# Performance work log

Measured on AMD Instinct MI355X. Metric: run time of the kernel, lower is better.

## Reference

```python
import jax, jax.numpy as jnp
import numpy as np

N_NODES = 100000
N_EDGES = 1600000
NUM_FEATURES = 128
NUM_CLASSES = 10
NUM_GRAPHS = 64


def setup_inputs() -> dict:
    key = jax.random.key(0)
    ks = jax.random.split(key, 16)
    x = jax.random.normal(ks[0], (N_NODES, NUM_FEATURES), dtype=jnp.float32)
    edge_index = jax.random.randint(ks[1], (2, N_EDGES), 0, N_NODES, dtype=jnp.int64)
    batch = jnp.sort(jax.random.randint(ks[2], (N_NODES,), 0, NUM_GRAPHS, dtype=jnp.int64))

    def glorot(k, fan_in, fan_out):
        s = jnp.sqrt(6.0 / (fan_in + fan_out)).astype(jnp.float32)
        return jax.random.uniform(k, (fan_in, fan_out), jnp.float32, -s, s)

    dims = [(NUM_FEATURES, 128), (128, 128), (128, 128), (128, 64), (64, 32)]
    params = {}
    for i, (fi, fo) in enumerate(dims, start=1):
        params[f"W{i}"] = glorot(ks[2 + i], fi, fo)
        params[f"b{i}"] = jnp.zeros((fo,), jnp.float32)
    params["Wfc"] = glorot(ks[10], 32, NUM_CLASSES)
    params["bfc"] = jnp.zeros((NUM_CLASSES,), jnp.float32)
    return {"x": x, "edge_index": edge_index, "batch": batch, **params}


def reference(x, edge_index, batch, W1, b1, W2, b2, W3, b3, W4, b4, W5, b5, Wfc, bfc):
    N = x.shape[0]
    loops = jnp.arange(N, dtype=edge_index.dtype)
    src = jnp.concatenate([edge_index[0], loops])  # message source j
    dst = jnp.concatenate([edge_index[1], loops])  # message target i
    # GCN symmetric normalization: deg computed on targets incl. self loops
    deg = jax.ops.segment_sum(jnp.ones_like(dst, x.dtype), dst, num_segments=N)
    dinv = jnp.where(deg > 0, jax.lax.rsqrt(deg), 0.0)
    norm = (dinv[src] * dinv[dst])[:, None]  # [E+N, 1]

    def gcn_conv(h, W, b):
        h = h @ W  # transform first (smaller gather width when out < in)
        msg = h[src] * norm
        return jax.ops.segment_sum(msg, dst, num_segments=N) + b

    h = jax.nn.relu(gcn_conv(x, W1, b1))
    h = jax.nn.relu(gcn_conv(h, W2, b2))
    h = jax.nn.relu(gcn_conv(h, W3, b3))
    h = jax.nn.relu(gcn_conv(h, W4, b4))
    h = jax.nn.relu(gcn_conv(h, W5, b5))

    # global_mean_pool over graph membership
    sums = jax.ops.segment_sum(h, batch, num_segments=NUM_GRAPHS)
    cnts = jax.ops.segment_sum(jnp.ones((N,), h.dtype), batch, num_segments=NUM_GRAPHS)
    pooled = sums / jnp.maximum(cnts, 1.0)[:, None]

    # dropout is identity in eval mode
    return pooled @ Wfc + bfc
```

## Files before the change

### kernel.cpp

```cpp
#include <hip/hip_runtime.h>
#include <hip/hip_bf16.h>

#define N_NODES 100000
#define N_EDGES 1600000
#define N_GRAPHS 64
#define WNB 192
#define BCAP 64

typedef __attribute__((ext_vector_type(8))) short bf16x8;
typedef __attribute__((ext_vector_type(4))) float f32x4;

__device__ inline float bflo(unsigned u) { return __uint_as_float(u << 16); }
__device__ inline float bfhi(unsigned u) { return __uint_as_float(u & 0xffff0000u); }
__device__ inline unsigned short f2bf(float f) {
    unsigned u = __float_as_uint(f);
    return (unsigned short)((u + 0x7fff + ((u >> 16) & 1)) >> 16);
}


__global__ __launch_bounds__(256) void k_setup(int* __restrict__ cursor, int n,
                                               const float* __restrict__ W1,
                                               const float* __restrict__ W2,
                                               const float* __restrict__ W3,
                                               const float* __restrict__ W4,
                                               const float* __restrict__ W5,
                                               unsigned short* __restrict__ wt1,
                                               unsigned short* __restrict__ wt2,
                                               unsigned short* __restrict__ wt3,
                                               unsigned short* __restrict__ wt4,
                                               unsigned short* __restrict__ wt5) {
    const int nb = (N_NODES + 255) / 256;
    if ((int)blockIdx.x < nb) {
        int i = blockIdx.x * 256 + threadIdx.x;
        if (i < n) cursor[i] = i * BCAP;
        return;
    }
    int i = (blockIdx.x - nb) * 256 + threadIdx.x;
    const float* W; unsigned short* WT; int FI, FO, j;
    if (i < 16384)      { W = W1; WT = wt1; FI = 128; FO = 128; j = i; }
    else if (i < 32768) { W = W2; WT = wt2; FI = 128; FO = 128; j = i - 16384; }
    else if (i < 49152) { W = W3; WT = wt3; FI = 128; FO = 128; j = i - 32768; }
    else if (i < 57344) { W = W4; WT = wt4; FI = 128; FO = 64;  j = i - 49152; }
    else if (i < 59392) { W = W5; WT = wt5; FI = 64;  FO = 32;  j = i - 57344; }
    else return;
    int n_ = j / FI, k_ = j % FI;
    WT[j] = f2bf(W[(size_t)k_ * FO + n_]);
}


__global__ __launch_bounds__(256) void k_fillw(const int* __restrict__ ei,
                                               int* __restrict__ cursor,
                                               int* __restrict__ cols, int e) {
    const int w = blockIdx.x & 7;
    const int b = blockIdx.x >> 3;
    const int lo = w * 12500, hi = lo + 12500;
    const int4* d4 = (const int4*)(ei + e);
    const int n4 = e >> 2;
    for (int i = b * 256 + threadIdx.x; i < n4; i += WNB * 256) {
        int4 d = d4[i];
        int base = 4 * i;
        if (d.x >= lo && d.x < hi) {
            int p = atomicAdd(&cursor[d.x], 1);
            if (p < d.x * BCAP + BCAP) cols[p] = ei[base];
        }
        if (d.y >= lo && d.y < hi) {
            int p = atomicAdd(&cursor[d.y], 1);
            if (p < d.y * BCAP + BCAP) cols[p] = ei[base + 1];
        }
        if (d.z >= lo && d.z < hi) {
            int p = atomicAdd(&cursor[d.z], 1);
            if (p < d.z * BCAP + BCAP) cols[p] = ei[base + 2];
        }
        if (d.w >= lo && d.w < hi) {
            int p = atomicAdd(&cursor[d.w], 1);
            if (p < d.w * BCAP + BCAP) cols[p] = ei[base + 3];
        }
    }
}


template <int FA> struct rowvec {};
template <> struct rowvec<128> { using V = uint4; };
template <> struct rowvec<64>  { using V = uint2; };
template <> struct rowvec<32>  { using V = unsigned; };

__device__ inline void upacc(uint4 u, float* a) {
    a[0] += bflo(u.x); a[1] += bfhi(u.x); a[2] += bflo(u.y); a[3] += bfhi(u.y);
    a[4] += bflo(u.z); a[5] += bfhi(u.z); a[6] += bflo(u.w); a[7] += bfhi(u.w);
}
__device__ inline void upacc(uint2 u, float* a) {
    a[0] += bflo(u.x); a[1] += bfhi(u.x); a[2] += bflo(u.y); a[3] += bfhi(u.y);
}
__device__ inline void upacc(unsigned u, float* a) {
    a[0] += bflo(u); a[1] += bfhi(u);
}

template <int FA>
__device__ inline void gather(const unsigned short* __restrict__ T,
                              const int* __restrict__ cursor,
                              const int* __restrict__ cols,
                              int node, int li, float* acc) {
    using V = typename rowvec<FA>::V;
    constexpr int NF = FA / 16;
    const V* Tp = reinterpret_cast<const V*>(T);

    #pragma unroll
    for (int k = 0; k < NF; k++) acc[k] = 0.f;

    V us = Tp[(size_t)node * 16 + li];
    upacc(us, acc);

    const int e0 = node * BCAP;
    int deg = cursor[node] - e0;
    if (deg > BCAP) deg = BCAP;
    const int nch = deg >> 2;

    int4 c0 = {0, 0, 0, 0}, c1 = {0, 0, 0, 0};
    if (nch > 0) c0 = *reinterpret_cast<const int4*>(cols + e0);
    if (nch > 1) c1 = *reinterpret_cast<const int4*>(cols + e0 + 4);

    int e = e0;
    for (int it = 0; it < nch; ++it) {
        int4 cc = c0;
        c0 = c1;
        if (it + 2 < nch) c1 = *reinterpret_cast<const int4*>(cols + e + 8);
        V t0 = Tp[(size_t)cc.x * 16 + li];
        V t1 = Tp[(size_t)cc.y * 16 + li];
        V t2 = Tp[(size_t)cc.z * 16 + li];
        V t3 = Tp[(size_t)cc.w * 16 + li];
        upacc(t0, acc); upacc(t1, acc); upacc(t2, acc); upacc(t3, acc);
        e += 4;
    }
    for (int r = e0 + (nch << 2), rend = e0 + deg; r < rend; ++r) {
        int c = __builtin_nontemporal_load(cols + r);
        V t = Tp[(size_t)c * 16 + li];
        upacc(t, acc);
    }
}


template <int FI, int FO>
__global__ __launch_bounds__(256) void k_gemm1(const float* __restrict__ Ain,
                                               const unsigned short* __restrict__ WT,
                                               unsigned short* __restrict__ Tout,
                                               const int* __restrict__ cursor,
                                               float* __restrict__ dinv, int n) {
    constexpr int NT = FO / 16;
    constexpr int NC = FI / 32;
    __shared__ unsigned short tile[4][16][FO];
    __shared__ float sdv[64];
    const int row0b = blockIdx.x * 64;
    if (threadIdx.x < 64) {
        int r = row0b + threadIdx.x;
        int rc = r < n ? r : n - 1;
        float v = rsqrtf((float)(cursor[rc] - BCAP * rc + 1));
        sdv[threadIdx.x] = v;
        if (r < n) dinv[r] = v;
    }
    __syncthreads();

    const int wave = threadIdx.x >> 6;
    const int lane = threadIdx.x & 63;
    const int m = lane & 15;
    const int q = lane >> 4;
    const int row0 = row0b + wave * 16;
    int arow = row0 + m;
    if (arow > n - 1) arow = n - 1;

    f32x4 acc[NT];
    #pragma unroll
    for (int j = 0; j < NT; j++) acc[j] = (f32x4){0.f, 0.f, 0.f, 0.f};

    #pragma unroll
    for (int c = 0; c < NC; c++) {
        const int k0 = c * 32 + q * 8;
        const float* ap = Ain + (size_t)arow * FI + k0;
        float4 f0 = *reinterpret_cast<const float4*>(ap);
        float4 f1 = *reinterpret_cast<const float4*>(ap + 4);
        bf16x8 a;
        a[0] = (short)f2bf(f0.x); a[1] = (short)f2bf(f0.y);
        a[2] = (short)f2bf(f0.z); a[3] = (short)f2bf(f0.w);
        a[4] = (short)f2bf(f1.x); a[5] = (short)f2bf(f1.y);
        a[6] = (short)f2bf(f1.z); a[7] = (short)f2bf(f1.w);
        #pragma unroll
        for (int j = 0; j < NT; j++) {
            bf16x8 b = *reinterpret_cast<const bf16x8*>(
                           WT + (size_t)(j * 16 + m) * FI + k0);
            acc[j] = __builtin_amdgcn_mfma_f32_16x16x32_bf16(a, b, acc[j], 0, 0, 0);
        }
    }

    #pragma unroll
    for (int r = 0; r < 4; r++) {
        const float dv = sdv[wave * 16 + q * 4 + r];
        #pragma unroll
        for (int j = 0; j < NT; j++)
            tile[wave][q * 4 + r][j * 16 + m] = f2bf(acc[j][r] * dv);
    }

    constexpr int CPR = FO / 8;
    constexpr int ITERS = 16 * CPR / 64;
    #pragma unroll
    for (int it = 0; it < ITERS; it++) {
        int idx = it * 64 + lane;
        int rr = idx / CPR;
        int cc = idx % CPR;
        int row = row0 + rr;
        if (row < n) {
            uint4 v = *reinterpret_cast<const uint4*>(&tile[wave][rr][cc * 8]);
            *reinterpret_cast<uint4*>(&Tout[(size_t)row * FO + cc * 8]) = v;
        }
    }
}


template <int FA, int FB>
__global__ __launch_bounds__(256) void k_fused(const unsigned short* __restrict__ T,
                                               const int* __restrict__ cursor,
                                               const int* __restrict__ cols,
                                               const float* __restrict__ dinv,
                                               const float* __restrict__ bias,
                                               const unsigned short* __restrict__ WT,
                                               unsigned short* __restrict__ Tout, int n) {
    constexpr int NF = FA / 16;
    constexpr int STR = FA + 8;
    __shared__ unsigned short hrow[16][STR];
    __shared__ float sdv[16];

    const int w = threadIdx.x >> 6;
    const int lane = threadIdx.x & 63;
    const int sub = lane >> 4;
    const int li  = lane & 15;
    const int node0 = blockIdx.x * 16;
    const int r = w * 4 + sub;

    int node = node0 + r;
    const bool valid = node < n;
    if (!valid) node = n - 1;

    const float dn = dinv[node];
    float acc[NF];
    gather<FA>(T, cursor, cols, node, li, acc);

    {
        float b[NF];
        if constexpr (NF == 8) {
            float4 ba = reinterpret_cast<const float4*>(bias)[2 * li];
            float4 bb = reinterpret_cast<const float4*>(bias)[2 * li + 1];
            b[0] = ba.x; b[1] = ba.y; b[2] = ba.z; b[3] = ba.w;
            b[4] = bb.x; b[5] = bb.y; b[6] = bb.z; b[7] = bb.w;
        } else if constexpr (NF == 4) {
            float4 ba = reinterpret_cast<const float4*>(bias)[li];
            b[0] = ba.x; b[1] = ba.y; b[2] = ba.z; b[3] = ba.w;
        } else {
            float2 ba = reinterpret_cast<const float2*>(bias)[li];
            b[0] = ba.x; b[1] = ba.y;
        }
        unsigned pk[NF / 2];
        #pragma unroll
        for (int k = 0; k < NF / 2; k++) {
            float r0 = fmaxf(fmaf(dn, acc[2 * k], b[2 * k]), 0.f);
            float r1 = fmaxf(fmaf(dn, acc[2 * k + 1], b[2 * k + 1]), 0.f);
            pk[k] = (unsigned)f2bf(r0) | ((unsigned)f2bf(r1) << 16);
        }
        if constexpr (NF == 8)
            *reinterpret_cast<uint4*>(&hrow[r][li * 8]) =
                make_uint4(pk[0], pk[1], pk[2], pk[3]);
        else if constexpr (NF == 4)
            *reinterpret_cast<uint2*>(&hrow[r][li * 4]) = make_uint2(pk[0], pk[1]);
        else
            *reinterpret_cast<unsigned*>(&hrow[r][li * 2]) = pk[0];
        if (li == 0) sdv[r] = dn;
    }

    __syncthreads();

    constexpr int NTILES = FB / 16;
    constexpr int NC = FA / 32;
    const int m = lane & 15;
    const int q = lane >> 4;

    for (int j = w; j < NTILES; j += 4) {
        f32x4 a4 = (f32x4){0.f, 0.f, 0.f, 0.f};
        #pragma unroll
        for (int c = 0; c < NC; c++) {
            const int k0 = c * 32 + q * 8;
            bf16x8 a = *reinterpret_cast<const bf16x8*>(&hrow[m][k0]);
            bf16x8 b = *reinterpret_cast<const bf16x8*>(
                           WT + (size_t)(j * 16 + m) * FA + k0);
            a4 = __builtin_amdgcn_mfma_f32_16x16x32_bf16(a, b, a4, 0, 0, 0);
        }
        #pragma unroll
        for (int rr = 0; rr < 4; rr++) {
            int row = node0 + q * 4 + rr;
            if (row < n)
                Tout[(size_t)row * FB + j * 16 + m] = f2bf(a4[rr] * sdv[q * 4 + rr]);
        }
    }
}


template <int FA>
__global__ __launch_bounds__(256) void k_agg(const unsigned short* __restrict__ T,
                                             const int* __restrict__ cursor,
                                             const int* __restrict__ cols,
                                             const float* __restrict__ dinv,
                                             const float* __restrict__ bias,
                                             unsigned short* __restrict__ Hout, int n) {
    const int w = threadIdx.x >> 6;
    const int lane = threadIdx.x & 63;
    const int sub = lane >> 4;
    const int li  = lane & 15;

    int node = blockIdx.x * 16 + w * 4 + sub;
    const bool valid = node < n;
    if (!valid) node = n - 1;

    const float dn = dinv[node];
    float acc[FA / 16];
    gather<FA>(T, cursor, cols, node, li, acc);

    if (valid) {
        float2 b2 = reinterpret_cast<const float2*>(bias)[li];
        float r0 = fmaxf(fmaf(dn, acc[0], b2.x), 0.f);
        float r1 = fmaxf(fmaf(dn, acc[1], b2.y), 0.f);
        unsigned pk = (unsigned)f2bf(r0) | ((unsigned)f2bf(r1) << 16);
        reinterpret_cast<unsigned*>(Hout + (size_t)node * FA)[li] = pk;
    }
}


__global__ __launch_bounds__(256) void k_poolfc(const unsigned short* __restrict__ H,
                                                const int* __restrict__ batch,
                                                const float* __restrict__ Wfc,
                                                const float* __restrict__ bfc,
                                                float* __restrict__ out, int n) {
    __shared__ float red0[256], red1[256];
    __shared__ float pl[32];
    __shared__ int se[2];
    int g = blockIdx.x;
    int t = threadIdx.x;
    if (t < 2) {
        int target = g + t;
        int lo = 0, hi = n;
        while (lo < hi) {
            int mid = (lo + hi) >> 1;
            if (batch[mid] < target) lo = mid + 1; else hi = mid;
        }
        se[t] = lo;
    }
    __syncthreads();
    int s = se[0], e = se[1];
    int c = t & 15;
    int grp = t >> 4;
    float a0 = 0.f, a1 = 0.f;
    for (int i = s + grp; i < e; i += 16) {
        unsigned u = reinterpret_cast<const unsigned*>(H + (size_t)i * 32)[c];
        a0 += bflo(u); a1 += bfhi(u);
    }
    red0[t] = a0; red1[t] = a1;
    __syncthreads();
    for (int off = 128; off >= 16; off >>= 1) {
        if (t < off) { red0[t] += red0[t + off]; red1[t] += red1[t + off]; }
        __syncthreads();
    }
    if (t < 16) {
        float cnt = fmaxf((float)(e - s), 1.0f);
        pl[2 * t]     = red0[t] / cnt;
        pl[2 * t + 1] = red1[t] / cnt;
    }
    __syncthreads();
    if (t < 10) {
        float a = bfc[t];
        #pragma unroll
        for (int k = 0; k < 32; k++) a += pl[k] * Wfc[k * 10 + t];
        out[g * 10 + t] = a;
    }
}


extern "C" void kernel_launch(void* const* d_in, const int* in_sizes, int n_in,
                              void* d_out, int out_size, void* d_ws, size_t ws_size,
                              hipStream_t stream) {
    const int N = N_NODES, E = N_EDGES;

    const float* x     = (const float*)d_in[0];
    const int*   ei    = (const int*)d_in[1];
    const int*   batch = (const int*)d_in[2];
    const float* W1 = (const float*)d_in[3];  const float* b1 = (const float*)d_in[4];
    const float* W2 = (const float*)d_in[5];  const float* b2 = (const float*)d_in[6];
    const float* W3 = (const float*)d_in[7];  const float* b3 = (const float*)d_in[8];
    const float* W4 = (const float*)d_in[9];  const float* b4 = (const float*)d_in[10];
    const float* W5 = (const float*)d_in[11]; const float* b5 = (const float*)d_in[12];
    const float* Wfc = (const float*)d_in[13]; const float* bfc = (const float*)d_in[14];
    float* out = (float*)d_out;

    char* p = (char*)d_ws;
    auto take = [&](size_t b) { char* q = p; p += (b + 511) & ~(size_t)511; return q; };
    int*   cursor = (int*)take((size_t)N * 4);
    float* dinv   = (float*)take((size_t)N * 4);
    int*   cols   = (int*)take((size_t)N * BCAP * 4);
    unsigned short* wt1 = (unsigned short*)take(128 * 128 * 2);
    unsigned short* wt2 = (unsigned short*)take(128 * 128 * 2);
    unsigned short* wt3 = (unsigned short*)take(128 * 128 * 2);
    unsigned short* wt4 = (unsigned short*)take(128 * 64 * 2);
    unsigned short* wt5 = (unsigned short*)take(64 * 32 * 2);
    unsigned short* Ta  = (unsigned short*)take((size_t)N * 128 * 2);
    unsigned short* Tb  = (unsigned short*)take((size_t)N * 128 * 2);

    const int nb = (N + 255) / 256;
    const int gemmb = (N + 63) / 64;
    const int fusedb = (N + 15) / 16;

    k_setup<<<nb + 232, 256, 0, stream>>>(cursor, N, W1, W2, W3, W4, W5,
                                          wt1, wt2, wt3, wt4, wt5);
    k_fillw<<<8 * WNB, 256, 0, stream>>>(ei, cursor, cols, E);

    k_gemm1<128, 128><<<gemmb, 256, 0, stream>>>(x, wt1, Ta, cursor, dinv, N);
    k_fused<128, 128><<<fusedb, 256, 0, stream>>>(Ta, cursor, cols, dinv, b1, wt2, Tb, N);
    k_fused<128, 128><<<fusedb, 256, 0, stream>>>(Tb, cursor, cols, dinv, b2, wt3, Ta, N);
    k_fused<128, 64><<<fusedb, 256, 0, stream>>>(Ta, cursor, cols, dinv, b3, wt4, Tb, N);
    k_fused<64, 32><<<fusedb, 256, 0, stream>>>(Tb, cursor, cols, dinv, b4, wt5, Ta, N);
    k_agg<32><<<fusedb, 256, 0, stream>>>(Ta, cursor, cols, dinv, b5, Tb, N);

    k_poolfc<<<N_GRAPHS, 256, 0, stream>>>(Tb, batch, Wfc, bfc, out, N);
}
```

Baseline: 538.9 us.

## Sort nodes by degree via counting sort to balance gather work per block

Adds a histogram, scan and scatter pass that builds a permutation of nodes ordered by in-degree. The fused and aggregation kernels then process nodes through this permutation, so each wave's 4 nodes have similar neighbour counts and less divergence or idle lanes in the gather loop. In exchange it adds three small kernel launches, a serial single-block scan, and scattered output row writes and less locality between neighbouring nodes.

```diff
diff --git a/kernel.cpp b/kernel.cpp
--- a/kernel.cpp
+++ b/kernel.cpp
@@ -6,6 +6,7 @@
 #define N_GRAPHS 64
 #define WNB 192
 #define BCAP 64
+#define NHB ((N_NODES + 255) / 256)
 
 typedef __attribute__((ext_vector_type(8))) short bf16x8;
 typedef __attribute__((ext_vector_type(4))) float f32x4;
@@ -75,6 +76,61 @@
             int p = atomicAdd(&cursor[d.w], 1);
             if (p < d.w * BCAP + BCAP) cols[p] = ei[base + 3];
         }
+    }
+}
+
+
+__global__ __launch_bounds__(256) void k_hist(const int* __restrict__ cursor,
+                                              int* __restrict__ counts, int n) {
+    __shared__ int h[BCAP + 1];
+    if (threadIdx.x <= BCAP) h[threadIdx.x] = 0;
+    __syncthreads();
+    int i = blockIdx.x * 256 + threadIdx.x;
+    if (i < n) {
+        int deg = cursor[i] - i * BCAP;
+        if (deg > BCAP) deg = BCAP;
+        atomicAdd(&h[deg], 1);
+    }
+    __syncthreads();
+    if (threadIdx.x <= BCAP) counts[threadIdx.x * NHB + blockIdx.x] = h[threadIdx.x];
+}
+
+__global__ __launch_bounds__(256) void k_scan(int* __restrict__ counts) {
+    __shared__ int tot[BCAP + 1], st[BCAP + 1];
+    int t = threadIdx.x;
+    if (t <= BCAP) {
+        int s = 0;
+        for (int b = 0; b < NHB; b++) s += counts[t * NHB + b];
+        tot[t] = s;
+    }
+    __syncthreads();
+    if (t == 0) {
+        int run = 0;
+        for (int b = 0; b <= BCAP; b++) { st[b] = run; run += tot[b]; }
+    }
+    __syncthreads();
+    if (t <= BCAP) {
+        int run = st[t];
+        for (int b = 0; b < NHB; b++) {
+            int c = counts[t * NHB + b];
+            counts[t * NHB + b] = run;
+            run += c;
+        }
+    }
+}
+
+__global__ __launch_bounds__(256) void k_scatter(const int* __restrict__ cursor,
+                                                 const int* __restrict__ counts,
+                                                 int* __restrict__ perm, int n) {
+    __shared__ int h[BCAP + 1];
+    if (threadIdx.x <= BCAP) h[threadIdx.x] = counts[threadIdx.x * NHB + blockIdx.x];
+    __syncthreads();
+    int i = blockIdx.x * 256 + threadIdx.x;
+    if (i < n) {
+        int deg = cursor[i] - i * BCAP;
+        if (deg > BCAP) deg = BCAP;
+        int pos = atomicAdd(&h[deg], 1);
+        perm[pos] = i;
     }
 }
 
@@ -218,6 +274,7 @@
 __global__ __launch_bounds__(256) void k_fused(const unsigned short* __restrict__ T,
                                                const int* __restrict__ cursor,
                                                const int* __restrict__ cols,
+                                               const int* __restrict__ perm,
                                                const float* __restrict__ dinv,
                                                const float* __restrict__ bias,
                                                const unsigned short* __restrict__ WT,
@@ -226,6 +283,7 @@
     constexpr int STR = FA + 8;
     __shared__ unsigned short hrow[16][STR];
     __shared__ float sdv[16];
+    __shared__ int snode[16];
 
     const int w = threadIdx.x >> 6;
     const int lane = threadIdx.x & 63;
@@ -234,9 +292,9 @@
     const int node0 = blockIdx.x * 16;
     const int r = w * 4 + sub;
 
-    int node = node0 + r;
-    const bool valid = node < n;
-    if (!valid) node = n - 1;
+    const int slot = node0 + r;
+    const bool valid = slot < n;
+    const int node = perm[valid ? slot : n - 1];
 
     const float dn = dinv[node];
     float acc[NF];
@@ -270,7 +328,7 @@
             *reinterpret_cast<uint2*>(&hrow[r][li * 4]) = make_uint2(pk[0], pk[1]);
         else
             *reinterpret_cast<unsigned*>(&hrow[r][li * 2]) = pk[0];
-        if (li == 0) sdv[r] = dn;
+        if (li == 0) { sdv[r] = dn; snode[r] = node; }
     }
 
     __syncthreads();
@@ -292,9 +350,10 @@
         }
         #pragma unroll
         for (int rr = 0; rr < 4; rr++) {
-            int row = node0 + q * 4 + rr;
-            if (row < n)
-                Tout[(size_t)row * FB + j * 16 + m] = f2bf(a4[rr] * sdv[q * 4 + rr]);
+            int sl = q * 4 + rr;
+            if (node0 + sl < n)
+                Tout[(size_t)snode[sl] * FB + j * 16 + m] =
+                    f2bf(a4[rr] * sdv[sl]);
         }
     }
 }
@@ -304,6 +363,7 @@
 __global__ __launch_bounds__(256) void k_agg(const unsigned short* __restrict__ T,
                                              const int* __restrict__ cursor,
                                              const int* __restrict__ cols,
+                                             const int* __restrict__ perm,
                                              const float* __restrict__ dinv,
                                              const float* __restrict__ bias,
                                              unsigned short* __restrict__ Hout, int n) {
@@ -312,9 +372,9 @@
     const int sub = lane >> 4;
     const int li  = lane & 15;
 
-    int node = blockIdx.x * 16 + w * 4 + sub;
-    const bool valid = node < n;
-    if (!valid) node = n - 1;
+    const int slot = blockIdx.x * 16 + w * 4 + sub;
+    const bool valid = slot < n;
+    const int node = perm[valid ? slot : n - 1];
 
     const float dn = dinv[node];
     float acc[FA / 16];
@@ -400,6 +460,8 @@
     int*   cursor = (int*)take((size_t)N * 4);
     float* dinv   = (float*)take((size_t)N * 4);
     int*   cols   = (int*)take((size_t)N * BCAP * 4);
+    int*   perm   = (int*)take((size_t)N * 4);
+    int*   counts = (int*)take((size_t)(BCAP + 1) * NHB * 4);
     unsigned short* wt1 = (unsigned short*)take(128 * 128 * 2);
     unsigned short* wt2 = (unsigned short*)take(128 * 128 * 2);
     unsigned short* wt3 = (unsigned short*)take(128 * 128 * 2);
@@ -416,12 +478,16 @@
                                           wt1, wt2, wt3, wt4, wt5);
     k_fillw<<<8 * WNB, 256, 0, stream>>>(ei, cursor, cols, E);
 
+    k_hist<<<NHB, 256, 0, stream>>>(cursor, counts, N);
+    k_scan<<<1, 256, 0, stream>>>(counts);
+    k_scatter<<<NHB, 256, 0, stream>>>(cursor, counts, perm, N);
+
     k_gemm1<128, 128><<<gemmb, 256, 0, stream>>>(x, wt1, Ta, cursor, dinv, N);
-    k_fused<128, 128><<<fusedb, 256, 0, stream>>>(Ta, cursor, cols, dinv, b1, wt2, Tb, N);
-    k_fused<128, 128><<<fusedb, 256, 0, stream>>>(Tb, cursor, cols, dinv, b2, wt3, Ta, N);
-    k_fused<128, 64><<<fusedb, 256, 0, stream>>>(Ta, cursor, cols, dinv, b3, wt4, Tb, N);
-    k_fused<64, 32><<<fusedb, 256, 0, stream>>>(Tb, cursor, cols, dinv, b4, wt5, Ta, N);
-    k_agg<32><<<fusedb, 256, 0, stream>>>(Ta, cursor, cols, dinv, b5, Tb, N);
+    k_fused<128, 128><<<fusedb, 256, 0, stream>>>(Ta, cursor, cols, perm, dinv, b1, wt2, Tb, N);
+    k_fused<128, 128><<<fusedb, 256, 0, stream>>>(Tb, cursor, cols, perm, dinv, b2, wt3, Ta, N);
+    k_fused<128, 64><<<fusedb, 256, 0, stream>>>(Ta, cursor, cols, perm, dinv, b3, wt4, Tb, N);
+    k_fused<64, 32><<<fusedb, 256, 0, stream>>>(Tb, cursor, cols, perm, dinv, b4, wt5, Ta, N);
+    k_agg<32><<<fusedb, 256, 0, stream>>>(Ta, cursor, cols, perm, dinv, b5, Tb, N);
 
     k_poolfc<<<N_GRAPHS, 256, 0, stream>>>(Tb, batch, Wfc, bfc, out, N);
 }
```

Result: slower. 550.9 us (+2.2%).

## Simplify CSR fill to one-pass atomics and widen 128-feature gather unrolling

Applied to the files above, without the earlier changes.

The windowed CSR bucket fill, where each of 8 destination ranges rescanned all edges, is replaced by a single pass. Each thread now handles four edges and reads source and destination as int4 vectors. This removes 8x redundant reads of the edge list but gives up the locality of the atomics that the windowing provided. A specialized 128-wide gather issues 8 neighbor row loads per iteration, with a 4-edge and scalar tail, to raise memory-level parallelism. The fused kernels also get a launch_bounds occupancy hint of 8, which may limit registers.

```diff
diff --git a/kernel.cpp b/kernel.cpp
--- a/kernel.cpp
+++ b/kernel.cpp
@@ -4,7 +4,6 @@
 #define N_NODES 100000
 #define N_EDGES 1600000
 #define N_GRAPHS 64
-#define WNB 192
 #define BCAP 64
 
 typedef __attribute__((ext_vector_type(8))) short bf16x8;
@@ -48,34 +47,21 @@
 }
 
 
-__global__ __launch_bounds__(256) void k_fillw(const int* __restrict__ ei,
+__global__ __launch_bounds__(256) void k_fill1(const int* __restrict__ ei,
                                                int* __restrict__ cursor,
                                                int* __restrict__ cols, int e) {
-    const int w = blockIdx.x & 7;
-    const int b = blockIdx.x >> 3;
-    const int lo = w * 12500, hi = lo + 12500;
     const int4* d4 = (const int4*)(ei + e);
+    const int4* s4 = (const int4*)ei;
     const int n4 = e >> 2;
-    for (int i = b * 256 + threadIdx.x; i < n4; i += WNB * 256) {
-        int4 d = d4[i];
-        int base = 4 * i;
-        if (d.x >= lo && d.x < hi) {
-            int p = atomicAdd(&cursor[d.x], 1);
-            if (p < d.x * BCAP + BCAP) cols[p] = ei[base];
-        }
-        if (d.y >= lo && d.y < hi) {
-            int p = atomicAdd(&cursor[d.y], 1);
-            if (p < d.y * BCAP + BCAP) cols[p] = ei[base + 1];
-        }
-        if (d.z >= lo && d.z < hi) {
-            int p = atomicAdd(&cursor[d.z], 1);
-            if (p < d.z * BCAP + BCAP) cols[p] = ei[base + 2];
-        }
-        if (d.w >= lo && d.w < hi) {
-            int p = atomicAdd(&cursor[d.w], 1);
-            if (p < d.w * BCAP + BCAP) cols[p] = ei[base + 3];
-        }
-    }
+    int i = blockIdx.x * 256 + threadIdx.x;
+    if (i >= n4) return;
+    int4 d = d4[i];
+    int4 s = s4[i];
+    int p;
+    p = atomicAdd(&cursor[d.x], 1); if (p < d.x * BCAP + BCAP) cols[p] = s.x;
+    p = atomicAdd(&cursor[d.y], 1); if (p < d.y * BCAP + BCAP) cols[p] = s.y;
+    p = atomicAdd(&cursor[d.z], 1); if (p < d.z * BCAP + BCAP) cols[p] = s.z;
+    p = atomicAdd(&cursor[d.w], 1); if (p < d.w * BCAP + BCAP) cols[p] = s.w;
 }
 
 
@@ -134,6 +120,63 @@
     for (int r = e0 + (nch << 2), rend = e0 + deg; r < rend; ++r) {
         int c = __builtin_nontemporal_load(cols + r);
         V t = Tp[(size_t)c * 16 + li];
+        upacc(t, acc);
+    }
+}
+
+__device__ inline void gather128(const unsigned short* __restrict__ T,
+                                 const int* __restrict__ cursor,
+                                 const int* __restrict__ cols,
+                                 int node, int li, float* acc) {
+    const uint4* Tp = reinterpret_cast<const uint4*>(T);
+    #pragma unroll
+    for (int k = 0; k < 8; k++) acc[k] = 0.f;
+
+    uint4 us = Tp[(size_t)node * 16 + li];
+
+    const int e0 = node * BCAP;
+    int deg = cursor[node] - e0;
+    if (deg > BCAP) deg = BCAP;
+    const int nch = deg >> 3;
+
+    int4 ca0 = {0, 0, 0, 0}, ca1 = {0, 0, 0, 0};
+    if (nch > 0) {
+        ca0 = *reinterpret_cast<const int4*>(cols + e0);
+        ca1 = *reinterpret_cast<const int4*>(cols + e0 + 4);
+    }
+    upacc(us, acc);
+
+    int e = e0;
+    for (int it = 0; it < nch; ++it) {
+        int4 c0 = ca0, c1 = ca1;
+        uint4 t0 = Tp[(size_t)c0.x * 16 + li];
+        uint4 t1 = Tp[(size_t)c0.y * 16 + li];
+        uint4 t2 = Tp[(size_t)c0.z * 16 + li];
+        uint4 t3 = Tp[(size_t)c0.w * 16 + li];
+        uint4 t4 = Tp[(size_t)c1.x * 16 + li];
+        uint4 t5 = Tp[(size_t)c1.y * 16 + li];
+        uint4 t6 = Tp[(size_t)c1.z * 16 + li];
+        uint4 t7 = Tp[(size_t)c1.w * 16 + li];
+        if (it + 1 < nch) {
+            ca0 = *reinterpret_cast<const int4*>(cols + e + 8);
+            ca1 = *reinterpret_cast<const int4*>(cols + e + 12);
+        }
+        upacc(t0, acc); upacc(t1, acc); upacc(t2, acc); upacc(t3, acc);
+        upacc(t4, acc); upacc(t5, acc); upacc(t6, acc); upacc(t7, acc);
+        e += 8;
+    }
+    if (deg & 4) {
+        int4 c0 = *reinterpret_cast<const int4*>(cols + e);
+        uint4 t0 = Tp[(size_t)c0.x * 16 + li];
+        uint4 t1 = Tp[(size_t)c0.y * 16 + li];
+        uint4 t2 = Tp[(size_t)c0.z * 16 + li];
+        uint4 t3 = Tp[(size_t)c0.w * 16 + li];
+        upacc(t0, acc); upacc(t1, acc); upacc(t2, acc); upacc(t3, acc);
+        e += 4;
+    }
+    for (int rend = e0 + deg; e < rend; ++e) {
+        int c = __builtin_nontemporal_load(cols + e);
+        uint4 t = Tp[(size_t)c * 16 + li];
         upacc(t, acc);
     }
 }
@@ -215,7 +258,7 @@
 
 
 template <int FA, int FB>
-__global__ __launch_bounds__(256) void k_fused(const unsigned short* __restrict__ T,
+__global__ __launch_bounds__(256, 8) void k_fused(const unsigned short* __restrict__ T,
                                                const int* __restrict__ cursor,
                                                const int* __restrict__ cols,
                                                const float* __restrict__ dinv,
@@ -240,7 +283,8 @@
 
     const float dn = dinv[node];
     float acc[NF];
-    gather<FA>(T, cursor, cols, node, li, acc);
+    if constexpr (FA == 128) gather128(T, cursor, cols, node, li, acc);
+    else                     gather<FA>(T, cursor, cols, node, li, acc);
 
     {
         float b[NF];
@@ -411,10 +455,11 @@
     const int nb = (N + 255) / 256;
     const int gemmb = (N + 63) / 64;
     const int fusedb = (N + 15) / 16;
+    const int fillb = ((E >> 2) + 255) / 256;
 
     k_setup<<<nb + 232, 256, 0, stream>>>(cursor, N, W1, W2, W3, W4, W5,
                                           wt1, wt2, wt3, wt4, wt5);
-    k_fillw<<<8 * WNB, 256, 0, stream>>>(ei, cursor, cols, E);
+    k_fill1<<<fillb, 256, 0, stream>>>(ei, cursor, cols, E);
 
     k_gemm1<128, 128><<<gemmb, 256, 0, stream>>>(x, wt1, Ta, cursor, dinv, N);
     k_fused<128, 128><<<fusedb, 256, 0, stream>>>(Ta, cursor, cols, dinv, b1, wt2, Tb, N);
```

Measured after the change: 704.9 us. 1.31x slower.
